# Performance work log

Measured on AMD Instinct MI355X. Metric: run time of the kernel, lower is better.

Reference implementation:

```python
import jax, jax.numpy as jnp
import numpy as np

D = 512    # d_model == EMBED_DIM
H = 8      # nhead
FF = 2048  # dim_feedforward
T, B, S, M = 64, 32, 64, 256
EPS = 1e-5


def setup_inputs() -> dict:
    key = jax.random.key(0)
    ks = iter(jax.random.split(key, 40))
    rn = lambda k, shp, s=0.02: s * jax.random.normal(k, shp, jnp.float32)
    inp = {
        'tgt': jax.random.normal(next(ks), (T, B, D), jnp.float32),
        'memory': jax.random.normal(next(ks), (M, B, D), jnp.float32),
        'semantics': jax.random.normal(next(ks), (B, S, D), jnp.float32),
    }
    for pfx in ('pt', 'sa', 'ca'):  # pre_target, self_attn, cross multihead_attn
        inp[pfx + '_wqkv'] = rn(next(ks), (3 * D, D))
        inp[pfx + '_bqkv'] = jnp.zeros((3 * D,), jnp.float32)
        inp[pfx + '_wo'] = rn(next(ks), (D, D))
        inp[pfx + '_bo'] = jnp.zeros((D,), jnp.float32)
    # relevant_mlp_pre_target: fc0 (2D->D), relu, fc1 (D->D), relu, fc2 (D->1)
    inp['mlp_w0'] = rn(next(ks), (D, 2 * D), float(np.sqrt(2.0 / (2 * D))))
    inp['mlp_b0'] = jnp.zeros((D,), jnp.float32)
    inp['mlp_w1'] = rn(next(ks), (D, D), float(np.sqrt(2.0 / D)))
    inp['mlp_b1'] = jnp.zeros((D,), jnp.float32)
    inp['mlp_w2'] = rn(next(ks), (1, D), float(np.sqrt(2.0 / D)))
    inp['mlp_b2'] = jnp.zeros((1,), jnp.float32)
    inp['ffn_w1'] = rn(next(ks), (FF, D))
    inp['ffn_b1'] = jnp.zeros((FF,), jnp.float32)
    inp['ffn_w2'] = rn(next(ks), (D, FF))
    inp['ffn_b2'] = jnp.zeros((D,), jnp.float32)
    for i in (1, 2, 3):
        inp[f'ln{i}_g'] = jnp.ones((D,), jnp.float32)
        inp[f'ln{i}_b'] = jnp.zeros((D,), jnp.float32)
    return inp


def layernorm(x, g, b):
    mu = jnp.mean(x, -1, keepdims=True)
    var = jnp.var(x, -1, keepdims=True)
    return (x - mu) * jax.lax.rsqrt(var + EPS) * g + b


def mha(q, k, v, wqkv, bqkv, wo, bo):
    # q,k,v: (L, B, D) seq-first, like torch nn.MultiheadAttention
    hd = D // H
    wq, wk, wv = jnp.split(wqkv, 3, axis=0)
    bq, bk, bv = jnp.split(bqkv, 3)
    qh = (q @ wq.T + bq).reshape(q.shape[0], q.shape[1], H, hd)
    kh = (k @ wk.T + bk).reshape(k.shape[0], k.shape[1], H, hd)
    vh = (v @ wv.T + bv).reshape(v.shape[0], v.shape[1], H, hd)
    scale = 1.0 / float(np.sqrt(hd))
    att = jax.nn.softmax(jnp.einsum('qbhd,kbhd->bhqk', qh * scale, kh), axis=-1)
    out = jnp.einsum('bhqk,kbhd->qbhd', att, vh).reshape(q.shape[0], q.shape[1], D)
    return out @ wo.T + bo


def get_relevant_semantic(feats, sem, w0, b0, w1, b1, w2, b2):
    # feats: (B,T,D), sem: (B,S,D). Linear-on-concat == sum of two linears, so we
    # never materialize the (B,T,S,2D) cat tensor; hidden (B,T,S,D) is unavoidable math.
    w0c, w0s = w0[:, :D], w0[:, D:]
    h = (feats @ w0c.T)[:, :, None, :] + (sem @ w0s.T)[:, None, :, :] + b0  # (B,T,S,D)
    h = jax.nn.relu(h)
    h = jax.nn.relu(h @ w1.T + b1)
    scores = h @ w2.T + b2                      # (B,T,S,1)
    a = jax.nn.softmax(scores, axis=2)          # softmax over sem axis
    return jnp.sum(sem[:, None, :, :] * a, axis=2)  # (B,T,D)


def reference(tgt, memory, semantics,
              pt_wqkv, pt_bqkv, pt_wo, pt_bo,
              sa_wqkv, sa_bqkv, sa_wo, sa_bo,
              ca_wqkv, ca_bqkv, ca_wo, ca_bo,
              mlp_w0, mlp_b0, mlp_w1, mlp_b1, mlp_w2, mlp_b2,
              ffn_w1, ffn_b1, ffn_w2, ffn_b2,
              ln1_g, ln1_b, ln2_g, ln2_b, ln3_g, ln3_b):
    # MULTIHEAD_PRE_TARGET branch (eval mode: dropout = identity)
    rel = get_relevant_semantic(jnp.transpose(tgt, (1, 0, 2)), semantics,
                                mlp_w0, mlp_b0, mlp_w1, mlp_b1, mlp_w2, mlp_b2)
    sem_k = jnp.transpose(rel, (1, 0, 2))  # (T,B,D) seq-first key/value
    x = tgt + mha(tgt, sem_k, sem_k, pt_wqkv, pt_bqkv, pt_wo, pt_bo)
    # self attention
    x = layernorm(x + mha(x, x, x, sa_wqkv, sa_bqkv, sa_wo, sa_bo), ln1_g, ln1_b)
    # cross attention over encoder memory
    x = layernorm(x + mha(x, memory, memory, ca_wqkv, ca_bqkv, ca_wo, ca_bo), ln2_g, ln2_b)
    # feed-forward
    ff = jax.nn.relu(x @ ffn_w1.T + ffn_b1) @ ffn_w2.T + ffn_b2
    return layernorm(x + ff, ln3_g, ln3_b)
```

## Files before the change

kernel.cpp:

```cpp
#include <hip/hip_runtime.h>
#include <hip/hip_bf16.h>

#define WS_B 32

typedef __attribute__((ext_vector_type(8))) __bf16 bf16x8;
typedef __attribute__((ext_vector_type(4))) float f32x4;
typedef unsigned short ushort_t;

#define MB(x) ((size_t)(x) << 20)

__device__ __forceinline__ unsigned packpair(float lo, float hi) {
    return ((__float_as_uint(lo) + 0x8000u) >> 16) |
           ((__float_as_uint(hi) + 0x8000u) & 0xffff0000u);
}
__device__ __forceinline__ ushort_t f2bf(float x) {
    return (ushort_t)((__float_as_uint(x) + 0x8000u) >> 16);
}
__device__ __forceinline__ float bf2f(ushort_t u) {
    return __uint_as_float(((unsigned)u) << 16);
}
__device__ __forceinline__ unsigned fuse_word(unsigned f, unsigned s) {
    float lo = __uint_as_float(f << 16) + __uint_as_float(s << 16);
    float hi = __uint_as_float(f & 0xffff0000u) + __uint_as_float(s & 0xffff0000u);
    lo = fmaxf(lo, 0.f);
    hi = fmaxf(hi, 0.f);
    return packpair(lo, hi);
}

struct CvtArgs {
    const float* src[13];
    ushort_t* dst[13];
    int n4[13];
};
__global__ __launch_bounds__(256) void megacvt_kernel(CvtArgs a) {
    const int t = blockIdx.y;
    const int n = a.n4[t];
    const float4* S = (const float4*)a.src[t];
    uint2* D = (uint2*)a.dst[t];
    for (int i = blockIdx.x * 256 + threadIdx.x; i < n; i += gridDim.x * 256) {
        float4 v = S[i];
        uint2 o;
        o.x = packpair(v.x, v.y);
        o.y = packpair(v.z, v.w);
        D[i] = o;
    }
}

struct GemmDesc {
    const ushort_t* A;
    const ushort_t* W;
    const float* bias;
    const float* resid;
    float* C;
    ushort_t* Cb;
    int lda, ldw, ldc, K, relu, nbx, blkStart;
};
struct GemmBatch {
    GemmDesc d[4];
    int nd;
};

__global__ __launch_bounds__(256, 3) void mfma_gemm2(GemmBatch bt) {
    __shared__ ushort_t As[128 * 32];
    __shared__ ushort_t Bs[128 * 32];
    int di = 0;
#pragma unroll
    for (int i = 1; i < 4; ++i)
        if (i < bt.nd && (int)blockIdx.x >= bt.d[i].blkStart) di = i;
    const GemmDesc g = bt.d[di];
    const int local = blockIdx.x - g.blkStart;
    const int mb = local / g.nbx;
    const int nb = local - mb * g.nbx;

    const int tid = threadIdx.x;
    const int w = tid >> 6, lane = tid & 63;
    const int wm = w & 1, wn = w >> 1;
    const int l15 = lane & 15, quad = lane >> 4;

    const int arow = tid >> 1;
    const int a16 = (tid & 1) * 16;
    const ushort_t* Ap = g.A + (long)(mb * 128 + arow) * g.lda + a16;
    const ushort_t* Bp = g.W + (long)(nb * 128 + arow) * g.ldw + a16;
    ushort_t* Asw = &As[arow * 32 + a16];
    ushort_t* Bsw = &Bs[arow * 32 + a16];

    f32x4 acc[4][4];
#pragma unroll
    for (int i = 0; i < 4; ++i)
#pragma unroll
        for (int j = 0; j < 4; ++j) acc[i][j] = (f32x4)0.f;

    uint4 a0 = *(const uint4*)Ap;
    uint4 a1 = *(const uint4*)(Ap + 8);
    uint4 b0 = *(const uint4*)Bp;
    uint4 b1 = *(const uint4*)(Bp + 8);

    for (int k0 = 0; k0 < g.K; k0 += 32) {
        __syncthreads();
        *(uint4*)Asw = a0; *(uint4*)(Asw + 8) = a1;
        *(uint4*)Bsw = b0; *(uint4*)(Bsw + 8) = b1;
        if (k0 + 32 < g.K) {
            a0 = *(const uint4*)(Ap + k0 + 32);
            a1 = *(const uint4*)(Ap + k0 + 40);
            b0 = *(const uint4*)(Bp + k0 + 32);
            b1 = *(const uint4*)(Bp + k0 + 40);
        }
        __syncthreads();
        bf16x8 af[4], bf[4];
#pragma unroll
        for (int mt = 0; mt < 4; ++mt)
            af[mt] = *(const bf16x8*)&As[(wm * 64 + mt * 16 + l15) * 32 + quad * 8];
#pragma unroll
        for (int nt = 0; nt < 4; ++nt)
            bf[nt] = *(const bf16x8*)&Bs[(wn * 64 + nt * 16 + l15) * 32 + quad * 8];
#pragma unroll
        for (int mt = 0; mt < 4; ++mt)
#pragma unroll
            for (int nt = 0; nt < 4; ++nt)
                acc[mt][nt] = __builtin_amdgcn_mfma_f32_16x16x32_bf16(
                    af[mt], bf[nt], acc[mt][nt], 0, 0, 0);
    }

#pragma unroll
    for (int nt = 0; nt < 4; ++nt) {
        const int col = nb * 128 + wn * 64 + nt * 16 + l15;
        const float bv = g.bias ? g.bias[col] : 0.f;
#pragma unroll
        for (int mt = 0; mt < 4; ++mt) {
            const int row0 = mb * 128 + wm * 64 + mt * 16 + quad * 4;
#pragma unroll
            for (int rg = 0; rg < 4; ++rg) {
                float v = acc[mt][nt][rg] + bv;
                if (g.relu) v = fmaxf(v, 0.f);
                const long off = (long)(row0 + rg) * g.ldc + col;
                if (g.resid) v += g.resid[off];
                if (g.C) g.C[off] = v;
                if (g.Cb) g.Cb[off] = f2bf(v);
            }
        }
    }
}

__global__ __launch_bounds__(128, 3) void mfma_gemm3(GemmBatch bt) {
    __shared__ ushort_t As[64 * 32];
    __shared__ ushort_t Bs[128 * 32];
    int di = 0;
#pragma unroll
    for (int i = 1; i < 4; ++i)
        if (i < bt.nd && (int)blockIdx.x >= bt.d[i].blkStart) di = i;
    const GemmDesc g = bt.d[di];
    const int local = blockIdx.x - g.blkStart;
    const int mb = local / g.nbx;
    const int nb = local - mb * g.nbx;

    const int tid = threadIdx.x;
    const int wn = tid >> 6, lane = tid & 63;
    const int l15 = lane & 15, quad = lane >> 4;

    const int ar = tid >> 1, ac = (tid & 1) * 16;
    const ushort_t* Ap = g.A + (long)(mb * 64 + ar) * g.lda + ac;
    const ushort_t* Bp = g.W + (long)(nb * 128 + tid) * g.ldw;
    ushort_t* Asw = &As[ar * 32 + ac];
    ushort_t* Bsw = &Bs[tid * 32];

    f32x4 acc[4][4];
#pragma unroll
    for (int i = 0; i < 4; ++i)
#pragma unroll
        for (int j = 0; j < 4; ++j) acc[i][j] = (f32x4)0.f;

    uint4 a0 = *(const uint4*)Ap;
    uint4 a1 = *(const uint4*)(Ap + 8);
    uint4 b0 = *(const uint4*)Bp;
    uint4 b1 = *(const uint4*)(Bp + 8);
    uint4 b2 = *(const uint4*)(Bp + 16);
    uint4 b3 = *(const uint4*)(Bp + 24);

    for (int k0 = 0; k0 < g.K; k0 += 32) {
        __syncthreads();
        *(uint4*)Asw = a0; *(uint4*)(Asw + 8) = a1;
        *(uint4*)Bsw = b0; *(uint4*)(Bsw + 8) = b1;
        *(uint4*)(Bsw + 16) = b2; *(uint4*)(Bsw + 24) = b3;
        if (k0 + 32 < g.K) {
            a0 = *(const uint4*)(Ap + k0 + 32);
            a1 = *(const uint4*)(Ap + k0 + 40);
            b0 = *(const uint4*)(Bp + k0 + 32);
            b1 = *(const uint4*)(Bp + k0 + 40);
            b2 = *(const uint4*)(Bp + k0 + 48);
            b3 = *(const uint4*)(Bp + k0 + 56);
        }
        __syncthreads();
        bf16x8 af[4], bf[4];
#pragma unroll
        for (int mt = 0; mt < 4; ++mt)
            af[mt] = *(const bf16x8*)&As[(mt * 16 + l15) * 32 + quad * 8];
#pragma unroll
        for (int nt = 0; nt < 4; ++nt)
            bf[nt] = *(const bf16x8*)&Bs[(wn * 64 + nt * 16 + l15) * 32 + quad * 8];
#pragma unroll
        for (int mt = 0; mt < 4; ++mt)
#pragma unroll
            for (int nt = 0; nt < 4; ++nt)
                acc[mt][nt] = __builtin_amdgcn_mfma_f32_16x16x32_bf16(
                    af[mt], bf[nt], acc[mt][nt], 0, 0, 0);
    }

#pragma unroll
    for (int nt = 0; nt < 4; ++nt) {
        const int col = nb * 128 + wn * 64 + nt * 16 + l15;
        const float bv = g.bias ? g.bias[col] : 0.f;
#pragma unroll
        for (int mt = 0; mt < 4; ++mt) {
            const int row0 = mb * 64 + mt * 16 + quad * 4;
#pragma unroll
            for (int rg = 0; rg < 4; ++rg) {
                float v = acc[mt][nt][rg] + bv;
                if (g.relu) v = fmaxf(v, 0.f);
                const long off = (long)(row0 + rg) * g.ldc + col;
                if (g.resid) v += g.resid[off];
                if (g.C) g.C[off] = v;
                if (g.Cb) g.Cb[off] = f2bf(v);
            }
        }
    }
}

__global__ __launch_bounds__(512, 2) void h2score_kernel(
    const ushort_t* __restrict__ Fb,
    const ushort_t* __restrict__ Sb,
    const ushort_t* __restrict__ w1b,
    const float* __restrict__ b1,
    const float* __restrict__ w2,
    float* __restrict__ scores4)
{
    __shared__ ushort_t As[128 * 32];
    __shared__ ushort_t Bs[256 * 32];
    __shared__ float scred[128 * 4];
    const int tid = threadIdx.x;
    const int mb = blockIdx.x, nb = blockIdx.y;
    const int w = tid >> 6, lane = tid & 63;
    const int wm = w & 1, wn = w >> 1;
    const int l15 = lane & 15, quad = lane >> 4;

    const int arow = tid >> 2, akc = tid & 3;
    const int m_g = mb * 128 + arow;
    const int r = m_g >> 6, s = m_g & 63, bidx = r & 31;
    const ushort_t* Fp = Fb + (long)r * 512 + akc * 8;
    const ushort_t* Sp = Sb + (long)(bidx * 64 + s) * 512 + akc * 8;
    const ushort_t* Bp0 = w1b + (long)(nb * 256 + arow) * 512 + akc * 8;
    const ushort_t* Bp1 = Bp0 + (long)128 * 512;
    ushort_t* Asw = &As[arow * 32 + akc * 8];
    ushort_t* Bsw0 = &Bs[arow * 32 + akc * 8];
    ushort_t* Bsw1 = Bsw0 + 128 * 32;

    f32x4 acc[4][4];
#pragma unroll
    for (int i = 0; i < 4; ++i)
#pragma unroll
        for (int j = 0; j < 4; ++j) acc[i][j] = (f32x4)0.f;

    for (int k0 = 0; k0 < 512; k0 += 32) {
        uint4 fa = *(const uint4*)(Fp + k0);
        uint4 sa = *(const uint4*)(Sp + k0);
        uint4 bb0 = *(const uint4*)(Bp0 + k0);
        uint4 bb1 = *(const uint4*)(Bp1 + k0);
        __syncthreads();
        uint4 o;
        o.x = fuse_word(fa.x, sa.x);
        o.y = fuse_word(fa.y, sa.y);
        o.z = fuse_word(fa.z, sa.z);
        o.w = fuse_word(fa.w, sa.w);
        *(uint4*)Asw = o;
        *(uint4*)Bsw0 = bb0;
        *(uint4*)Bsw1 = bb1;
        __syncthreads();
        bf16x8 af[4], bf[4];
#pragma unroll
        for (int mt = 0; mt < 4; ++mt)
            af[mt] = *(const bf16x8*)&As[(wm * 64 + mt * 16 + l15) * 32 + quad * 8];
#pragma unroll
        for (int nt = 0; nt < 4; ++nt)
            bf[nt] = *(const bf16x8*)&Bs[(wn * 64 + nt * 16 + l15) * 32 + quad * 8];
#pragma unroll
        for (int mt = 0; mt < 4; ++mt)
#pragma unroll
            for (int nt = 0; nt < 4; ++nt)
                acc[mt][nt] = __builtin_amdgcn_mfma_f32_16x16x32_bf16(
                    af[mt], bf[nt], acc[mt][nt], 0, 0, 0);
    }
    __syncthreads();

    float sp[4][4];
#pragma unroll
    for (int mt = 0; mt < 4; ++mt)
#pragma unroll
        for (int rg = 0; rg < 4; ++rg) sp[mt][rg] = 0.f;
#pragma unroll
    for (int nt = 0; nt < 4; ++nt) {
        const int col = nb * 256 + wn * 64 + nt * 16 + l15;
        const float cb = b1[col];
        const float cw = w2[col];
#pragma unroll
        for (int mt = 0; mt < 4; ++mt) {
#pragma unroll
            for (int rg = 0; rg < 4; ++rg)
                sp[mt][rg] += fmaxf(acc[mt][nt][rg] + cb, 0.f) * cw;
        }
    }
#pragma unroll
    for (int mt = 0; mt < 4; ++mt)
#pragma unroll
        for (int rg = 0; rg < 4; ++rg) {
            float v = sp[mt][rg];
            v += __shfl_xor(v, 1);
            v += __shfl_xor(v, 2);
            v += __shfl_xor(v, 4);
            v += __shfl_xor(v, 8);
            if (l15 == 0)
                scred[(wm * 64 + mt * 16 + quad * 4 + rg) * 4 + wn] = v;
        }
    __syncthreads();
    if (tid < 128) {
        float t = scred[tid * 4] + scred[tid * 4 + 1]
                + scred[tid * 4 + 2] + scred[tid * 4 + 3];
        scores4[(long)nb * 131072 + mb * 128 + tid] = t;
    }
}

__global__ __launch_bounds__(256) void softrel_kernel(
    const float* __restrict__ sc4,
    const ushort_t* __restrict__ semb,
    ushort_t* __restrict__ rel)
{
    __shared__ float a_s[64];
    const int tid = threadIdx.x;
    const int r = blockIdx.x;
    const int b = r & (WS_B - 1);
    if (tid < 64) {
        float t = sc4[r * 64 + tid] + sc4[131072 + r * 64 + tid];
        float m = t;
#pragma unroll
        for (int off = 32; off > 0; off >>= 1) m = fmaxf(m, __shfl_xor(m, off));
        float e = __expf(t - m);
        float su = e;
#pragma unroll
        for (int off = 32; off > 0; off >>= 1) su += __shfl_xor(su, off);
        a_s[tid] = e / su;
    }
    __syncthreads();
#pragma unroll
    for (int dd = 0; dd < 2; ++dd) {
        const int d = tid + dd * 256;
        float accd = 0.f;
        const ushort_t* sp = semb + (long)b * 64 * 512 + d;
        for (int s = 0; s < 64; ++s)
            accd += a_s[s] * bf2f(sp[s * 512]);
        rel[(long)r * 512 + d] = f2bf(accd);
    }
}

__global__ __launch_bounds__(256) void attn2_kernel(
    const ushort_t* __restrict__ Qm, int ldq, int qoff,
    const ushort_t* __restrict__ Km, int ldk, int koff,
    const ushort_t* __restrict__ Vm, int ldv, int voff,
    ushort_t* __restrict__ O,
    int Lk)
{
    __shared__ float sQT[64 * 34];
    __shared__ float sKT[64 * 68];
    __shared__ float sS[32 * 260];
    __shared__ float sredm[8 * 34];
    __shared__ float sreds[8 * 34];
    const int tid = threadIdx.x;
    const int b  = blockIdx.x >> 4;
    const int h  = (blockIdx.x >> 1) & 7;
    const int qt = blockIdx.x & 1;
    const int L8 = Lk >> 3;

    {
        const int q = tid >> 3, c = tid & 7;
        const int qg = qt * 32 + q;
        const ushort_t* pp = Qm + (long)(qg * WS_B + b) * ldq + qoff + h * 64 + c * 8;
        uint4 u = *(const uint4*)pp;
        const ushort_t* us = (const ushort_t*)&u;
#pragma unroll
        for (int i = 0; i < 8; ++i)
            sQT[(c * 8 + i) * 34 + q] = bf2f(us[i]);
    }

    const int k4 = (tid & 15) * 4;
    const int q2 = (tid >> 4) * 2;

    for (int kt = 0; kt < Lk; kt += 64) {
        __syncthreads();
        {
            const int kk = tid >> 3, c = tid & 7;
#pragma unroll
            for (int half = 0; half < 2; ++half) {
                const int kr = kk + half * 32;
                const ushort_t* pp = Km + (long)((kt + kr) * WS_B + b) * ldk + koff + h * 64 + c * 8;
                uint4 u = *(const uint4*)pp;
                const ushort_t* us = (const ushort_t*)&u;
#pragma unroll
                for (int i = 0; i < 8; ++i)
                    sKT[(c * 8 + i) * 68 + kr] = bf2f(us[i]);
            }
        }
        __syncthreads();
        float acc[2][4] = {{0.f, 0.f, 0.f, 0.f}, {0.f, 0.f, 0.f, 0.f}};
        for (int d = 0; d < 64; ++d) {
            const float qa = sQT[d * 34 + q2];
            const float qb = sQT[d * 34 + q2 + 1];
            const float4 kv = *(const float4*)&sKT[d * 68 + k4];
            acc[0][0] += qa * kv.x; acc[0][1] += qa * kv.y;
            acc[0][2] += qa * kv.z; acc[0][3] += qa * kv.w;
            acc[1][0] += qb * kv.x; acc[1][1] += qb * kv.y;
            acc[1][2] += qb * kv.z; acc[1][3] += qb * kv.w;
        }
#pragma unroll
        for (int i = 0; i < 2; ++i) {
            float4 v;
            v.x = acc[i][0] * 0.125f; v.y = acc[i][1] * 0.125f;
            v.z = acc[i][2] * 0.125f; v.w = acc[i][3] * 0.125f;
            *(float4*)&sS[(q2 + i) * 260 + kt + k4] = v;
        }
    }
    __syncthreads();

    {
        const int q = tid & 31, part = tid >> 5;
        const int kb = part * L8;
        float m = -1e30f;
        for (int k = 0; k < L8; ++k) m = fmaxf(m, sS[q * 260 + kb + k]);
        sredm[part * 34 + q] = m;
        __syncthreads();
        float M = sredm[q];
#pragma unroll
        for (int pz = 1; pz < 8; ++pz) M = fmaxf(M, sredm[pz * 34 + q]);
        float su = 0.f;
        for (int k = 0; k < L8; ++k) {
            float e = __expf(sS[q * 260 + kb + k] - M);
            sS[q * 260 + kb + k] = e;
            su += e;
        }
        sreds[part * 34 + q] = su;
    }
    __syncthreads();

    const int d4 = (tid & 15) * 4;
    float o[2][4] = {{0.f, 0.f, 0.f, 0.f}, {0.f, 0.f, 0.f, 0.f}};
    float* sV = sKT;
    for (int kt = 0; kt < Lk; kt += 64) {
        __syncthreads();
        {
            const int kk = tid >> 3, c = tid & 7;
#pragma unroll
            for (int half = 0; half < 2; ++half) {
                const int kr = kk + half * 32;
                const ushort_t* pp = Vm + (long)((kt + kr) * WS_B + b) * ldv + voff + h * 64 + c * 8;
                uint4 u = *(const uint4*)pp;
                const ushort_t* us = (const ushort_t*)&u;
                float4 w0, w1;
                w0.x = bf2f(us[0]); w0.y = bf2f(us[1]);
                w0.z = bf2f(us[2]); w0.w = bf2f(us[3]);
                w1.x = bf2f(us[4]); w1.y = bf2f(us[5]);
                w1.z = bf2f(us[6]); w1.w = bf2f(us[7]);
                *(float4*)&sV[kr * 68 + c * 8] = w0;
                *(float4*)&sV[kr * 68 + c * 8 + 4] = w1;
            }
        }
        __syncthreads();
        for (int k = 0; k < 64; ++k) {
            const float p0 = sS[q2 * 260 + kt + k];
            const float p1 = sS[(q2 + 1) * 260 + kt + k];
            const float4 vv = *(const float4*)&sV[k * 68 + d4];
            o[0][0] += p0 * vv.x; o[0][1] += p0 * vv.y;
            o[0][2] += p0 * vv.z; o[0][3] += p0 * vv.w;
            o[1][0] += p1 * vv.x; o[1][1] += p1 * vv.y;
            o[1][2] += p1 * vv.z; o[1][3] += p1 * vv.w;
        }
    }

#pragma unroll
    for (int i = 0; i < 2; ++i) {
        float su = 0.f;
#pragma unroll
        for (int pz = 0; pz < 8; ++pz) su += sreds[pz * 34 + q2 + i];
        const float inv = 1.f / su;
        const int qg = qt * 32 + q2 + i;
        ushort_t* op = O + (long)(qg * WS_B + b) * 512 + h * 64 + d4;
        uint2 pk;
        pk.x = packpair(o[i][0] * inv, o[i][1] * inv);
        pk.y = packpair(o[i][2] * inv, o[i][3] * inv);
        *(uint2*)op = pk;
    }
}

__global__ __launch_bounds__(256) void ln_kernel(
    const float* __restrict__ X,
    const float* __restrict__ g,
    const float* __restrict__ be,
    float* __restrict__ Y,
    ushort_t* __restrict__ Yb)
{
    const int row = blockIdx.x * 4 + (threadIdx.x >> 6);
    const int lane = threadIdx.x & 63;
    const float4* xp = (const float4*)(X + (long)row * 512);
    float4 x0 = xp[lane], x1 = xp[lane + 64];
    float sum = x0.x + x0.y + x0.z + x0.w + x1.x + x1.y + x1.z + x1.w;
    float sq = x0.x * x0.x + x0.y * x0.y + x0.z * x0.z + x0.w * x0.w
             + x1.x * x1.x + x1.y * x1.y + x1.z * x1.z + x1.w * x1.w;
#pragma unroll
    for (int off = 32; off > 0; off >>= 1) {
        sum += __shfl_xor(sum, off);
        sq += __shfl_xor(sq, off);
    }
    const float mu = sum * (1.f / 512.f);
    const float var = sq * (1.f / 512.f) - mu * mu;
    const float rs = rsqrtf(var + 1e-5f);
    const float4* gp = (const float4*)g;
    const float4* bp = (const float4*)be;
    float4 g0 = gp[lane], g1 = gp[lane + 64], b0 = bp[lane], b1 = bp[lane + 64];
    float4 y0, y1;
    y0.x = (x0.x - mu) * rs * g0.x + b0.x;
    y0.y = (x0.y - mu) * rs * g0.y + b0.y;
    y0.z = (x0.z - mu) * rs * g0.z + b0.z;
    y0.w = (x0.w - mu) * rs * g0.w + b0.w;
    y1.x = (x1.x - mu) * rs * g1.x + b1.x;
    y1.y = (x1.y - mu) * rs * g1.y + b1.y;
    y1.z = (x1.z - mu) * rs * g1.z + b1.z;
    y1.w = (x1.w - mu) * rs * g1.w + b1.w;
    float4* yp = (float4*)(Y + (long)row * 512);
    yp[lane] = y0; yp[lane + 64] = y1;
    if (Yb) {
        uint2* ybp = (uint2*)(Yb + (long)row * 512);
        uint2 p0, p1;
        p0.x = packpair(y0.x, y0.y); p0.y = packpair(y0.z, y0.w);
        p1.x = packpair(y1.x, y1.y); p1.y = packpair(y1.z, y1.w);
        ybp[lane] = p0; ybp[lane + 64] = p1;
    }
}

static inline GemmDesc mkdesc(const ushort_t* A, int lda, const ushort_t* W, int ldw,
                              const float* bias, const float* resid, float* C,
                              ushort_t* Cb, int ldc, int N, int K, int relu,
                              int blkStart)
{
    GemmDesc d;
    d.A = A; d.W = W; d.bias = bias; d.resid = resid; d.C = C; d.Cb = Cb;
    d.lda = lda; d.ldw = ldw; d.ldc = ldc; d.K = K; d.relu = relu;
    d.nbx = N / 128;
    d.blkStart = blkStart;
    return d;
}
static inline void mgemm3(hipStream_t s, const ushort_t* A, int lda,
                          const ushort_t* W, int ldw, const float* bias,
                          const float* resid, float* C, ushort_t* Cb,
                          int ldc, int M, int N, int K, bool relu)
{
    GemmBatch bt;
    bt.nd = 1;
    bt.d[0] = mkdesc(A, lda, W, ldw, bias, resid, C, Cb, ldc, N, K, relu ? 1 : 0, 0);
    bt.d[1] = bt.d[0]; bt.d[2] = bt.d[0]; bt.d[3] = bt.d[0];
    mfma_gemm3<<<(M / 64) * (N / 128), 128, 0, s>>>(bt);
}

extern "C" void kernel_launch(void* const* d_in, const int* in_sizes, int n_in,
                              void* d_out, int out_size, void* d_ws, size_t ws_size,
                              hipStream_t stream)
{
    (void)in_sizes; (void)n_in; (void)out_size; (void)ws_size;
    const float* tgt       = (const float*)d_in[0];
    const float* memory    = (const float*)d_in[1];
    const float* semantics = (const float*)d_in[2];
    const float* pt_wqkv   = (const float*)d_in[3];
    const float* pt_bqkv   = (const float*)d_in[4];
    const float* pt_wo     = (const float*)d_in[5];
    const float* pt_bo     = (const float*)d_in[6];
    const float* sa_wqkv   = (const float*)d_in[7];
    const float* sa_bqkv   = (const float*)d_in[8];
    const float* sa_wo     = (const float*)d_in[9];
    const float* sa_bo     = (const float*)d_in[10];
    const float* ca_wqkv   = (const float*)d_in[11];
    const float* ca_bqkv   = (const float*)d_in[12];
    const float* ca_wo     = (const float*)d_in[13];
    const float* ca_bo     = (const float*)d_in[14];
    const float* mlp_w0    = (const float*)d_in[15];
    const float* mlp_b0    = (const float*)d_in[16];
    const float* mlp_w1    = (const float*)d_in[17];
    const float* mlp_b1    = (const float*)d_in[18];
    const float* mlp_w2    = (const float*)d_in[19];
    const float* ffn_w1    = (const float*)d_in[21];
    const float* ffn_b1    = (const float*)d_in[22];
    const float* ffn_w2    = (const float*)d_in[23];
    const float* ffn_b2    = (const float*)d_in[24];
    const float* ln1_g     = (const float*)d_in[25];
    const float* ln1_b     = (const float*)d_in[26];
    const float* ln2_g     = (const float*)d_in[27];
    const float* ln2_b     = (const float*)d_in[28];
    const float* ln3_g     = (const float*)d_in[29];
    const float* ln3_b     = (const float*)d_in[30];

    char* p = (char*)d_ws;
    ushort_t* w0b   = (ushort_t*)(p + 0);
    ushort_t* w1b   = (ushort_t*)(p + MB(1));
    ushort_t* ptwb  = (ushort_t*)(p + 1572864);
    ushort_t* ptob  = (ushort_t*)(p + MB(3));
    ushort_t* sawb  = (ushort_t*)(p + 3670016);
    ushort_t* saob  = (ushort_t*)(p + MB(5));
    ushort_t* cawb  = (ushort_t*)(p + 5767168);
    ushort_t* caob  = (ushort_t*)(p + MB(7));
    ushort_t* f1b   = (ushort_t*)(p + 7864320);
    ushort_t* f2b   = (ushort_t*)(p + 9961472);
    ushort_t* memb  = (ushort_t*)(p + MB(12));
    ushort_t* cakvb = (ushort_t*)(p + MB(20));
    ushort_t* tgtb  = (ushort_t*)(p + MB(36));
    ushort_t* semb  = (ushort_t*)(p + MB(38));
    ushort_t* Fb    = (ushort_t*)(p + MB(40));
    ushort_t* Sb    = (ushort_t*)(p + MB(42));
    float*    scores4 = (float*)(p + MB(44));
    ushort_t* relb  = (ushort_t*)(p + MB(45));
    ushort_t* Ob    = (ushort_t*)(p + MB(47));
    float*    x1f   = (float*)(p + MB(49));
    ushort_t* ptqb  = (ushort_t*)(p + MB(53));
    ushort_t* ptkvb = (ushort_t*)(p + MB(14));
    ushort_t* x1b   = (ushort_t*)(p + MB(18));
    ushort_t* saqkvb= (ushort_t*)(p + MB(38));
    float*    yf    = (float*)(p + MB(12));
    float*    x2f   = (float*)(p + MB(16));
    ushort_t* x2b   = (ushort_t*)(p + MB(36));
    ushort_t* caqb  = (ushort_t*)(p + MB(44));
    float*    x3f   = (float*)(p + MB(40));
    ushort_t* x3b   = (ushort_t*)(p + MB(38));
    ushort_t* hb    = (ushort_t*)(p + MB(20));

    CvtArgs ca;
    ca.src[0]  = tgt;       ca.dst[0]  = tgtb;  ca.n4[0]  = 262144;
    ca.src[1]  = semantics; ca.dst[1]  = semb;  ca.n4[1]  = 262144;
    ca.src[2]  = memory;    ca.dst[2]  = memb;  ca.n4[2]  = 1048576;
    ca.src[3]  = mlp_w0;    ca.dst[3]  = w0b;   ca.n4[3]  = 131072;
    ca.src[4]  = mlp_w1;    ca.dst[4]  = w1b;   ca.n4[4]  = 65536;
    ca.src[5]  = pt_wqkv;   ca.dst[5]  = ptwb;  ca.n4[5]  = 196608;
    ca.src[6]  = pt_wo;     ca.dst[6]  = ptob;  ca.n4[6]  = 65536;
    ca.src[7]  = sa_wqkv;   ca.dst[7]  = sawb;  ca.n4[7]  = 196608;
    ca.src[8]  = sa_wo;     ca.dst[8]  = saob;  ca.n4[8]  = 65536;
    ca.src[9]  = ca_wqkv;   ca.dst[9]  = cawb;  ca.n4[9]  = 196608;
    ca.src[10] = ca_wo;     ca.dst[10] = caob;  ca.n4[10] = 65536;
    ca.src[11] = ffn_w1;    ca.dst[11] = f1b;   ca.n4[11] = 262144;
    ca.src[12] = ffn_w2;    ca.dst[12] = f2b;   ca.n4[12] = 262144;
    megacvt_kernel<<<dim3(1024, 13), 256, 0, stream>>>(ca);

    {
        GemmBatch bt;
        bt.nd = 4;
        bt.d[0] = mkdesc(memb, 512, cawb + 512 * 512, 512, ca_bqkv + 512, nullptr,
                         nullptr, cakvb, 1024, 1024, 512, 0, 0);
        bt.d[1] = mkdesc(tgtb, 512, w0b, 1024, mlp_b0, nullptr,
                         nullptr, Fb, 512, 512, 512, 0, 512);
        bt.d[2] = mkdesc(semb, 512, w0b + 512, 1024, nullptr, nullptr,
                         nullptr, Sb, 512, 512, 512, 0, 576);
        bt.d[3] = mkdesc(tgtb, 512, ptwb, 512, pt_bqkv, nullptr,
                         nullptr, ptqb, 512, 512, 512, 0, 640);
        mfma_gemm2<<<704, 256, 0, stream>>>(bt);
    }

    h2score_kernel<<<dim3(1024, 2), 512, 0, stream>>>(Fb, Sb, w1b, mlp_b1,
                                                      mlp_w2, scores4);
    softrel_kernel<<<2048, 256, 0, stream>>>(scores4, semb, relb);

    mgemm3(stream, relb, 512, ptwb + 512 * 512, 512, pt_bqkv + 512, nullptr,
           nullptr, ptkvb, 1024, 2048, 1024, 512, false);
    attn2_kernel<<<512, 256, 0, stream>>>(ptqb, 512, 0, ptkvb, 1024, 0,
                                          ptkvb, 1024, 512, Ob, 64);
    mgemm3(stream, Ob, 512, ptob, 512, pt_bo, tgt, x1f, x1b, 512,
           2048, 512, 512, false);

    mgemm3(stream, x1b, 512, sawb, 512, sa_bqkv, nullptr, nullptr, saqkvb, 1536,
           2048, 1536, 512, false);
    attn2_kernel<<<512, 256, 0, stream>>>(saqkvb, 1536, 0, saqkvb, 1536, 512,
                                          saqkvb, 1536, 1024, Ob, 64);
    mgemm3(stream, Ob, 512, saob, 512, sa_bo, x1f, yf, nullptr, 512,
           2048, 512, 512, false);
    ln_kernel<<<512, 256, 0, stream>>>(yf, ln1_g, ln1_b, x2f, x2b);

    mgemm3(stream, x2b, 512, cawb, 512, ca_bqkv, nullptr, nullptr, caqb, 512,
           2048, 512, 512, false);
    attn2_kernel<<<512, 256, 0, stream>>>(caqb, 512, 0, cakvb, 1024, 0,
                                          cakvb, 1024, 512, Ob, 256);
    mgemm3(stream, Ob, 512, caob, 512, ca_bo, x2f, yf, nullptr, 512,
           2048, 512, 512, false);
    ln_kernel<<<512, 256, 0, stream>>>(yf, ln2_g, ln2_b, x3f, x3b);

    mgemm3(stream, x3b, 512, f1b, 512, ffn_b1, nullptr, nullptr, hb, 2048,
           2048, 2048, 512, true);
    mgemm3(stream, hb, 2048, f2b, 2048, ffn_b2, x3f, yf, nullptr, 512,
           2048, 512, 2048, false);
    ln_kernel<<<512, 256, 0, stream>>>(yf, ln3_g, ln3_b, (float*)d_out, nullptr);
}
```

Before: 520.6 us.

## Fuse MLP score GEMM with softmax and weighted semantic sum per row

```diff
diff --git a/kernel.cpp b/kernel.cpp
--- a/kernel.cpp
+++ b/kernel.cpp
@@ -225,33 +225,31 @@
     }
 }
 
-__global__ __launch_bounds__(512, 2) void h2score_kernel(
+__global__ __launch_bounds__(512, 2) void h2rel2_kernel(
     const ushort_t* __restrict__ Fb,
     const ushort_t* __restrict__ Sb,
     const ushort_t* __restrict__ w1b,
     const float* __restrict__ b1,
     const float* __restrict__ w2,
-    float* __restrict__ scores4)
+    const ushort_t* __restrict__ semb,
+    ushort_t* __restrict__ relb)
 {
-    __shared__ ushort_t As[128 * 32];
-    __shared__ ushort_t Bs[256 * 32];
-    __shared__ float scred[128 * 4];
+    __shared__ ushort_t As[64 * 32];
+    __shared__ ushort_t Bs[512 * 32];
+    __shared__ float aw[64];
     const int tid = threadIdx.x;
-    const int mb = blockIdx.x, nb = blockIdx.y;
-    const int w = tid >> 6, lane = tid & 63;
-    const int wm = w & 1, wn = w >> 1;
+    const int r = blockIdx.x;
+    const int b = r & 31;
+    const int wn = tid >> 6, lane = tid & 63;
     const int l15 = lane & 15, quad = lane >> 4;
 
-    const int arow = tid >> 2, akc = tid & 3;
-    const int m_g = mb * 128 + arow;
-    const int r = m_g >> 6, s = m_g & 63, bidx = r & 31;
-    const ushort_t* Fp = Fb + (long)r * 512 + akc * 8;
-    const ushort_t* Sp = Sb + (long)(bidx * 64 + s) * 512 + akc * 8;
-    const ushort_t* Bp0 = w1b + (long)(nb * 256 + arow) * 512 + akc * 8;
-    const ushort_t* Bp1 = Bp0 + (long)128 * 512;
-    ushort_t* Asw = &As[arow * 32 + akc * 8];
-    ushort_t* Bsw0 = &Bs[arow * 32 + akc * 8];
-    ushort_t* Bsw1 = Bsw0 + 128 * 32;
+    const int arow = tid >> 3, akc = tid & 7;
+    const ushort_t* Fp = Fb + (long)r * 512 + akc * 4;
+    const ushort_t* Sp = Sb + (long)(b * 64 + arow) * 512 + akc * 4;
+    ushort_t* Asw = &As[arow * 32 + akc * 4];
+    const int brow = tid >> 2, bkc = tid & 3;
+    const ushort_t* Bp = w1b + (long)brow * 512 + bkc * 8;
+    ushort_t* Bsw = &Bs[brow * 32 + bkc * 8];
 
     f32x4 acc[4][4];
 #pragma unroll
@@ -260,24 +258,26 @@
         for (int j = 0; j < 4; ++j) acc[i][j] = (f32x4)0.f;
 
     for (int k0 = 0; k0 < 512; k0 += 32) {
-        uint4 fa = *(const uint4*)(Fp + k0);
-        uint4 sa = *(const uint4*)(Sp + k0);
-        uint4 bb0 = *(const uint4*)(Bp0 + k0);
-        uint4 bb1 = *(const uint4*)(Bp1 + k0);
-        __syncthreads();
-        uint4 o;
+        uint2 fa = *(const uint2*)(Fp + k0);
+        uint2 sa = *(const uint2*)(Sp + k0);
+        uint4 bb0 = *(const uint4*)(Bp + k0);
+        uint4 bb1 = *(const uint4*)(Bp + (long)128 * 512 + k0);
+        uint4 bb2 = *(const uint4*)(Bp + (long)256 * 512 + k0);
+        uint4 bb3 = *(const uint4*)(Bp + (long)384 * 512 + k0);
+        __syncthreads();
+        uint2 o;
         o.x = fuse_word(fa.x, sa.x);
         o.y = fuse_word(fa.y, sa.y);
-        o.z = fuse_word(fa.z, sa.z);
-        o.w = fuse_word(fa.w, sa.w);
-        *(uint4*)Asw = o;
-        *(uint4*)Bsw0 = bb0;
-        *(uint4*)Bsw1 = bb1;
+        *(uint2*)Asw = o;
+        *(uint4*)Bsw = bb0;
+        *(uint4*)(Bsw + 128 * 32) = bb1;
+        *(uint4*)(Bsw + 256 * 32) = bb2;
+        *(uint4*)(Bsw + 384 * 32) = bb3;
         __syncthreads();
         bf16x8 af[4], bf[4];
 #pragma unroll
         for (int mt = 0; mt < 4; ++mt)
-            af[mt] = *(const bf16x8*)&As[(wm * 64 + mt * 16 + l15) * 32 + quad * 8];
+            af[mt] = *(const bf16x8*)&As[(mt * 16 + l15) * 32 + quad * 8];
 #pragma unroll
         for (int nt = 0; nt < 4; ++nt)
             bf[nt] = *(const bf16x8*)&Bs[(wn * 64 + nt * 16 + l15) * 32 + quad * 8];
@@ -297,7 +297,7 @@
         for (int rg = 0; rg < 4; ++rg) sp[mt][rg] = 0.f;
 #pragma unroll
     for (int nt = 0; nt < 4; ++nt) {
-        const int col = nb * 256 + wn * 64 + nt * 16 + l15;
+        const int col = wn * 64 + nt * 16 + l15;
         const float cb = b1[col];
         const float cw = w2[col];
 #pragma unroll
@@ -307,6 +307,7 @@
                 sp[mt][rg] += fmaxf(acc[mt][nt][rg] + cb, 0.f) * cw;
         }
     }
+    float* scred = (float*)As;
 #pragma unroll
     for (int mt = 0; mt < 4; ++mt)
 #pragma unroll
@@ -317,45 +318,35 @@
             v += __shfl_xor(v, 4);
             v += __shfl_xor(v, 8);
             if (l15 == 0)
-                scred[(wm * 64 + mt * 16 + quad * 4 + rg) * 4 + wn] = v;
+                scred[(mt * 16 + quad * 4 + rg) * 8 + wn] = v;
         }
     __syncthreads();
-    if (tid < 128) {
-        float t = scred[tid * 4] + scred[tid * 4 + 1]
-                + scred[tid * 4 + 2] + scred[tid * 4 + 3];
-        scores4[(long)nb * 131072 + mb * 128 + tid] = t;
-    }
-}
-
-__global__ __launch_bounds__(256) void softrel_kernel(
-    const float* __restrict__ sc4,
-    const ushort_t* __restrict__ semb,
-    ushort_t* __restrict__ rel)
-{
-    __shared__ float a_s[64];
-    const int tid = threadIdx.x;
-    const int r = blockIdx.x;
-    const int b = r & (WS_B - 1);
+
     if (tid < 64) {
-        float t = sc4[r * 64 + tid] + sc4[131072 + r * 64 + tid];
-        float m = t;
-#pragma unroll
-        for (int off = 32; off > 0; off >>= 1) m = fmaxf(m, __shfl_xor(m, off));
-        float e = __expf(t - m);
+        const float* sc = scred + tid * 8;
+        float t = sc[0] + sc[1] + sc[2] + sc[3] + sc[4] + sc[5] + sc[6] + sc[7];
+        float mx = t;
+#pragma unroll
+        for (int off = 32; off > 0; off >>= 1) mx = fmaxf(mx, __shfl_xor(mx, off));
+        float e = __expf(t - mx);
         float su = e;
 #pragma unroll
         for (int off = 32; off > 0; off >>= 1) su += __shfl_xor(su, off);
-        a_s[tid] = e / su;
+        aw[tid] = e / su;
     }
     __syncthreads();
-#pragma unroll
-    for (int dd = 0; dd < 2; ++dd) {
-        const int d = tid + dd * 256;
-        float accd = 0.f;
-        const ushort_t* sp = semb + (long)b * 64 * 512 + d;
-        for (int s = 0; s < 64; ++s)
-            accd += a_s[s] * bf2f(sp[s * 512]);
-        rel[(long)r * 512 + d] = f2bf(accd);
+
+    if (tid < 256) {
+        const int d2 = tid * 2;
+        const ushort_t* sp2 = semb + (long)b * 64 * 512 + d2;
+        float a0 = 0.f, a1 = 0.f;
+        for (int s = 0; s < 64; ++s) {
+            const unsigned u = *(const unsigned*)(sp2 + s * 512);
+            const float wg = aw[s];
+            a0 += wg * __uint_as_float(u << 16);
+            a1 += wg * __uint_as_float(u & 0xffff0000u);
+        }
+        *(unsigned*)(relb + (long)r * 512 + d2) = packpair(a0, a1);
     }
 }
 
@@ -618,7 +609,6 @@
     ushort_t* semb  = (ushort_t*)(p + MB(38));
     ushort_t* Fb    = (ushort_t*)(p + MB(40));
     ushort_t* Sb    = (ushort_t*)(p + MB(42));
-    float*    scores4 = (float*)(p + MB(44));
     ushort_t* relb  = (ushort_t*)(p + MB(45));
     ushort_t* Ob    = (ushort_t*)(p + MB(47));
     float*    x1f   = (float*)(p + MB(49));
@@ -664,9 +654,8 @@
         mfma_gemm2<<<704, 256, 0, stream>>>(bt);
     }
 
-    h2score_kernel<<<dim3(1024, 2), 512, 0, stream>>>(Fb, Sb, w1b, mlp_b1,
-                                                      mlp_w2, scores4);
-    softrel_kernel<<<2048, 256, 0, stream>>>(scores4, semb, relb);
+    h2rel2_kernel<<<2048, 512, 0, stream>>>(Fb, Sb, w1b, mlp_b1, mlp_w2,
+                                            semb, relb);
 
     mgemm3(stream, relb, 512, ptwb + 512 * 512, 512, pt_bqkv + 512, nullptr,
            nullptr, ptkvb, 1024, 2048, 1024, 512, false);
```

Result: no change. 528.1 us (+1.5%).
